# Kernel tuning notes

Hardware: AMD Instinct MI355X
Metric: run time of the kernel (lower is better)

The kernel has to match this reference:

```python
import jax, jax.numpy as jnp
import numpy as np

N_NODES = 50000


def setup_inputs() -> dict:
    key = jax.random.key(0)
    k1, k2, k3 = jax.random.split(key, 3)
    x = jax.random.normal(k1, (N_NODES, 256), dtype=jnp.float32)
    edge_index = jax.random.randint(k2, (2, 1600000), 0, N_NODES, dtype=jnp.int64)
    W = jax.random.normal(k3, (256, 256), dtype=jnp.float32) / np.sqrt(256.0)
    b = jnp.zeros((256,), dtype=jnp.float32)
    return {"x": x, "edge_index": edge_index, "W": W, "b": b}


def reference(x, edge_index, W, b):
    # PyG GCNConv: add self-loops, symmetric normalization, linear, aggregate, bias; then ReLU.
    n = x.shape[0]
    self_loops = jnp.arange(n, dtype=edge_index.dtype)
    src = jnp.concatenate([edge_index[0], self_loops])  # [E+N]
    dst = jnp.concatenate([edge_index[1], self_loops])  # [E+N]

    # degree from incoming edges (incl. self loops)
    deg = jax.ops.segment_sum(jnp.ones_like(dst, dtype=x.dtype), dst, num_segments=n)
    dinv = jnp.where(deg > 0, jax.lax.rsqrt(deg), 0.0)
    norm = dinv[src] * dinv[dst]  # [E+N]

    xw = x @ W  # [N, out] linear first (GCNConv transforms then propagates)
    msgs = xw[src] * norm[:, None]  # gather + edge-normalize
    agg = jax.ops.segment_sum(msgs, dst, num_segments=n)  # scatter-add
    return jax.nn.relu(agg + b)
```

## Files before the change

kernel.cpp:

```cpp
#include <hip/hip_runtime.h>
#include <hip/hip_bf16.h>


#define FEATS 256
#define MAXBUCK 200
#define P1_CAP 64
#define BCAP 10240

typedef __bf16 bf16x8 __attribute__((ext_vector_type(8)));
typedef float f32x4 __attribute__((ext_vector_type(4)));

__device__ __forceinline__ unsigned short f2bf(float f) {
  unsigned u = __float_as_uint(f);
  u += 0x7fffu + ((u >> 16) & 1u);
  return (unsigned short)(u >> 16);
}
__device__ __forceinline__ float bflo(unsigned u) { return __uint_as_float(u << 16); }
__device__ __forceinline__ float bfhi(unsigned u) { return __uint_as_float(u & 0xFFFF0000u); }


__global__ __launch_bounds__(256) void zero_i32(int* __restrict__ p, int n) {
  int i = blockIdx.x * 256 + threadIdx.x;
  if (i < n) p[i] = 0;
}

__global__ __launch_bounds__(1024) void pass1_bin(const int* __restrict__ src,
                                                  const int* __restrict__ dst,
                                                  int E, int nbuck,
                                                  int* __restrict__ gcursor,
                                                  unsigned* __restrict__ temp) {
  __shared__ unsigned lbuf[MAXBUCK * P1_CAP];
  __shared__ int lcnt[MAXBUCK];
  __shared__ int lbase[MAXBUCK];
  const int tid = threadIdx.x;
  for (int i = tid; i < nbuck; i += 1024) lcnt[i] = 0;
  __syncthreads();

  const int e0 = blockIdx.x * 4096;
  #pragma unroll
  for (int i = 0; i < 4; ++i) {
    int e = e0 + i * 1024 + tid;
    if (e < E) {
      unsigned d = (unsigned)dst[e];
      unsigned p = (d << 16) | (unsigned)src[e];
      int b = (int)(d >> 8);
      int pos = atomicAdd(&lcnt[b], 1);
      if (pos < P1_CAP) {
        lbuf[b * P1_CAP + pos] = p;
      } else {
        int gp = atomicAdd(&gcursor[b], 1);
        temp[(size_t)b * BCAP + gp] = p;
      }
    }
  }
  __syncthreads();
  if (tid < nbuck) {
    int c = lcnt[tid]; if (c > P1_CAP) c = P1_CAP;
    lcnt[tid] = c;
    lbase[tid] = atomicAdd(&gcursor[tid], c);
  }
  __syncthreads();
  for (int i = tid; i < nbuck * P1_CAP; i += 1024) {
    int b = i >> 6, j = i & (P1_CAP - 1);
    if (j < lcnt[b]) temp[(size_t)b * BCAP + lbase[b] + j] = lbuf[i];
  }
}

__global__ __launch_bounds__(256) void scan_buckets(const int* __restrict__ gcursor,
                                                    int* __restrict__ bbase,
                                                    int* __restrict__ row_ptr,
                                                    int nbuck, int n) {
  __shared__ int tmp[256];
  int t = threadIdx.x;
  int v = (t < nbuck) ? min(gcursor[t], BCAP) : 0;
  tmp[t] = v;
  __syncthreads();
  #pragma unroll
  for (int off = 1; off < 256; off <<= 1) {
    int x = (t >= off) ? tmp[t - off] : 0;
    __syncthreads();
    tmp[t] += x;
    __syncthreads();
  }
  if (t < nbuck) bbase[t] = tmp[t] - v;
  if (t == 0) row_ptr[n] = tmp[255];
}

__global__ __launch_bounds__(1024) void pass2_csr(const unsigned* __restrict__ temp,
                                                  const int* __restrict__ gcursor,
                                                  const int* __restrict__ bbase,
                                                  unsigned short* __restrict__ csr16,
                                                  int* __restrict__ row_ptr,
                                                  float* __restrict__ dinv, int n) {
  __shared__ unsigned ebuf[BCAP];
  __shared__ unsigned short sorted[BCAP];
  __shared__ int hist[256], scn[256], sexcl[256], ofs[256];
  const int b = blockIdx.x;
  const int tid = threadIdx.x;
  int cnt = gcursor[b]; if (cnt > BCAP) cnt = BCAP;
  const int base = bbase[b];
  const unsigned* tp = temp + (size_t)b * BCAP;

  if (tid < 256) { hist[tid] = 0; ofs[tid] = 0; }
  for (int i = tid; i < cnt; i += 1024) ebuf[i] = tp[i];
  __syncthreads();
  for (int i = tid; i < cnt; i += 1024) atomicAdd(&hist[(ebuf[i] >> 16) & 255], 1);
  __syncthreads();

  if (tid < 256) scn[tid] = hist[tid];
  __syncthreads();
  #pragma unroll
  for (int off = 1; off < 256; off <<= 1) {
    int x = 0;
    if (tid < 256 && tid >= off) x = scn[tid - off];
    __syncthreads();
    if (tid < 256) scn[tid] += x;
    __syncthreads();
  }
  if (tid < 256) {
    int v = hist[tid];
    int excl = scn[tid] - v;
    sexcl[tid] = excl;
    int node = (b << 8) + tid;
    if (node < n) {
      row_ptr[node] = base + excl;
      dinv[node] = rsqrtf((float)(v + 1));
    }
  }
  __syncthreads();

  for (int i = tid; i < cnt; i += 1024) {
    unsigned e = ebuf[i];
    int dl = (int)((e >> 16) & 255);
    int pos = sexcl[dl] + atomicAdd(&ofs[dl], 1);
    sorted[pos] = (unsigned short)(e & 0xFFFFu);
  }
  __syncthreads();
  for (int i = tid; i < cnt; i += 1024) csr16[base + i] = sorted[i];
}


__global__ __launch_bounds__(256) void wt_build(const float* __restrict__ W,
                                                unsigned short* __restrict__ Wt) {
  int k = blockIdx.x;
  int nn = threadIdx.x;
  Wt[nn * FEATS + k] = f2bf(W[k * FEATS + nn]);
}


__global__ __launch_bounds__(256, 2) void gemm_mfma(const float* __restrict__ x,
                                                    const unsigned short* __restrict__ Wt,
                                                    const float* __restrict__ dinv,
                                                    unsigned short* __restrict__ xwp, int M) {
  __shared__ bf16x8 A_lds[32 * 64];
  __shared__ unsigned short C_lds[64 * 256];
  const int wv   = (int)(threadIdx.x >> 6);
  const int lane = (int)(threadIdx.x & 63);
  const int lm   = lane & 15;
  const int quad = lane >> 4;
  const int m0   = (int)blockIdx.x * 64;

  bf16x8 Bfrag[4][8];
  #pragma unroll
  for (int ct = 0; ct < 4; ++ct) {
    const unsigned short* wrow = Wt + (size_t)(wv * 64 + ct * 16 + lm) * FEATS + quad * 8;
    #pragma unroll
    for (int kc = 0; kc < 8; ++kc)
      Bfrag[ct][kc] = *(const bf16x8*)(wrow + kc * 32);
  }

  {
    int arow = m0 + wv * 16 + lm; if (arow >= M) arow = M - 1;
    const float* xrow = x + (size_t)arow * FEATS + quad * 8;
    #pragma unroll
    for (int kc = 0; kc < 8; ++kc) {
      const float4 f0 = *(const float4*)(xrow + kc * 32);
      const float4 f1 = *(const float4*)(xrow + kc * 32 + 4);
      union { bf16x8 v; unsigned short u[8]; } a;
      a.u[0] = f2bf(f0.x); a.u[1] = f2bf(f0.y); a.u[2] = f2bf(f0.z); a.u[3] = f2bf(f0.w);
      a.u[4] = f2bf(f1.x); a.u[5] = f2bf(f1.y); a.u[6] = f2bf(f1.z); a.u[7] = f2bf(f1.w);
      A_lds[(wv * 8 + kc) * 64 + lane] = a.v;
    }
  }
  __syncthreads();

  #pragma unroll
  for (int sub = 0; sub < 4; ++sub) {
    bf16x8 Af[8];
    #pragma unroll
    for (int kc = 0; kc < 8; ++kc) Af[kc] = A_lds[(sub * 8 + kc) * 64 + lane];

    f32x4 acc[4];
    #pragma unroll
    for (int ct = 0; ct < 4; ++ct) acc[ct] = (f32x4){0.f, 0.f, 0.f, 0.f};

    #pragma unroll
    for (int kc = 0; kc < 8; ++kc) {
      #pragma unroll
      for (int ct = 0; ct < 4; ++ct)
        acc[ct] = __builtin_amdgcn_mfma_f32_16x16x32_bf16(Af[kc], Bfrag[ct][kc], acc[ct], 0, 0, 0);
    }

    #pragma unroll
    for (int r = 0; r < 4; ++r) {
      const int lrow = sub * 16 + quad * 4 + r;
      int grow = m0 + lrow; if (grow >= M) grow = M - 1;
      const float dd = dinv[grow];
      #pragma unroll
      for (int ct = 0; ct < 4; ++ct)
        C_lds[lrow * 256 + wv * 64 + ((ct ^ quad) << 4) + lm] = f2bf(acc[ct][r] * dd);
    }
  }
  __syncthreads();

  const int t  = (int)(threadIdx.x & 31);
  const int r8 = (int)(threadIdx.x >> 5);
  #pragma unroll
  for (int j = 0; j < 8; ++j) {
    const int lrow = j * 8 + r8;
    const int grow = m0 + lrow;
    if (grow < M) {
      const int qr = (lrow >> 2) & 3;
      const unsigned short* srcp = C_lds + lrow * 256 + (((t * 16) ^ (qr << 5)) >> 1);
      *(uint4*)(xwp + (size_t)grow * FEATS + t * 8) = *(const uint4*)srcp;
    }
  }
}


__global__ __launch_bounds__(256) void aggregate(const unsigned short* __restrict__ xwp,
                                                 const float* __restrict__ dinv,
                                                 const int* __restrict__ row_ptr,
                                                 const unsigned short* __restrict__ csr16,
                                                 const float* __restrict__ bias,
                                                 float* __restrict__ out,
                                                 int n0, int n1) {
  const int node = n0 + (int)((blockIdx.x * blockDim.x + threadIdx.x) >> 6);
  const int lane = (int)(threadIdx.x & 63);
  if (node >= n1) return;
  const int co = lane << 2;

  uint2 sv = *(const uint2*)(xwp + (((size_t)node) << 8) + co);
  float4 acc;
  acc.x = bflo(sv.x); acc.y = bfhi(sv.x); acc.z = bflo(sv.y); acc.w = bfhi(sv.y);

  const int beg = row_ptr[node];
  const int end = row_ptr[node + 1];
  for (int base = beg; base < end; base += 64) {
    int idx = base + lane;
    int s = (idx < end) ? (int)csr16[idx] : 0;
    int m = end - base;
    if (m > 64) m = 64;
    int i = 0;
    for (; i + 8 <= m; i += 8) {
      uint2 v[8];
      #pragma unroll
      for (int j = 0; j < 8; ++j) {
        int sj = __shfl(s, i + j);
        v[j] = *(const uint2*)(xwp + (((size_t)sj) << 8) + co);
      }
      #pragma unroll
      for (int j = 0; j < 8; ++j) {
        acc.x += bflo(v[j].x); acc.y += bfhi(v[j].x);
        acc.z += bflo(v[j].y); acc.w += bfhi(v[j].y);
      }
    }
    for (; i < m; ++i) {
      int sj = __shfl(s, i);
      uint2 v = *(const uint2*)(xwp + (((size_t)sj) << 8) + co);
      acc.x += bflo(v.x); acc.y += bfhi(v.x);
      acc.z += bflo(v.y); acc.w += bfhi(v.y);
    }
  }

  const float dd = dinv[node];
  const float* bp = bias + co;
  f32x4 o;
  o.x = fmaxf(fmaf(acc.x, dd, bp[0]), 0.f);
  o.y = fmaxf(fmaf(acc.y, dd, bp[1]), 0.f);
  o.z = fmaxf(fmaf(acc.z, dd, bp[2]), 0.f);
  o.w = fmaxf(fmaf(acc.w, dd, bp[3]), 0.f);
  __builtin_nontemporal_store(o, (f32x4*)(out + (((size_t)node) << 8) + co));
}


extern "C" void kernel_launch(void* const* d_in, const int* in_sizes, int n_in,
                              void* d_out, int out_size, void* d_ws, size_t ws_size,
                              hipStream_t stream) {
  const float* x  = (const float*)d_in[0];
  const int*   ei = (const int*)d_in[1];
  const float* W  = (const float*)d_in[2];
  const float* b  = (const float*)d_in[3];

  const int n = in_sizes[0] / FEATS;
  const int E = in_sizes[1] / 2;
  const int* src = ei;
  const int* dst = ei + E;
  const int nbuck = (n + 255) >> 8;

  char* ws = (char*)d_ws;
  size_t o0 = 0;
  unsigned short* xwp    = (unsigned short*)(ws + o0); o0 += (size_t)n * 512;
  unsigned short* Wt     = (unsigned short*)(ws + o0); o0 += 131072;
  float*          dinv   = (float*)(ws + o0);          o0 += 200064;
  int*            row_ptr = (int*)(ws + o0);           o0 += 200064;
  unsigned short* csr16  = (unsigned short*)(ws + o0); o0 += 3200000;
  int*            gcursor = (int*)(ws + o0);           o0 += 1024;
  int*            bbase   = (int*)(ws + o0);           o0 += 1024;
  unsigned*       temp    = (unsigned*)(ws + o0);      o0 += (size_t)MAXBUCK * BCAP * 4;

  hipLaunchKernelGGL(zero_i32, dim3(1), dim3(256), 0, stream, gcursor, nbuck);
  hipLaunchKernelGGL(wt_build, dim3(256), dim3(256), 0, stream, W, Wt);

  const int g_p1 = (E + 4095) / 4096;
  hipLaunchKernelGGL(pass1_bin, dim3(g_p1), dim3(1024), 0, stream, src, dst, E, nbuck, gcursor, temp);
  hipLaunchKernelGGL(scan_buckets, dim3(1), dim3(256), 0, stream, gcursor, bbase, row_ptr, nbuck, n);
  hipLaunchKernelGGL(pass2_csr, dim3(nbuck), dim3(1024), 0, stream, temp, gcursor, bbase,
                     csr16, row_ptr, dinv, n);

  hipLaunchKernelGGL(gemm_mfma, dim3((n + 63) / 64), dim3(256), 0, stream, x, Wt, dinv, xwp, n);

  const int nh = (n + 1) >> 1;
  const int g_agg = (nh * 64 + 255) / 256;
  hipLaunchKernelGGL(aggregate, dim3(g_agg), dim3(256), 0, stream,
                     xwp, dinv, row_ptr, csr16, b, (float*)d_out, 0, nh);
  hipLaunchKernelGGL(aggregate, dim3(g_agg), dim3(256), 0, stream,
                     xwp, dinv, row_ptr, csr16, b, (float*)d_out, nh, n);
}
```

Baseline: 258.6 us.

## Gather two neighbor rows per wave with 16-byte loads and merge init kernels

The aggregate kernel now splits each wave into two 32-lane halves that each load a full 256-feature bf16 row with 16-byte loads, so one wave processes two edges per step. The halves are combined with a cross-half shuffle reduction. Out-of-range slots point at an extra zeroed padding row so loads need no branch. The zero and weight-transpose kernels are merged into one launch, and the two half-range aggregate launches become one. This aims to cut load instruction count and launch overhead, at the cost of extra shuffles, more registers and wasted loads on partial edge groups.

```diff
diff --git a/kernel.cpp b/kernel.cpp
--- a/kernel.cpp
+++ b/kernel.cpp
@@ -18,11 +18,6 @@
 __device__ __forceinline__ float bflo(unsigned u) { return __uint_as_float(u << 16); }
 __device__ __forceinline__ float bfhi(unsigned u) { return __uint_as_float(u & 0xFFFF0000u); }
 
-
-__global__ __launch_bounds__(256) void zero_i32(int* __restrict__ p, int n) {
-  int i = blockIdx.x * 256 + threadIdx.x;
-  if (i < n) p[i] = 0;
-}
 
 __global__ __launch_bounds__(1024) void pass1_bin(const int* __restrict__ src,
                                                   const int* __restrict__ dst,
@@ -140,11 +135,18 @@
 }
 
 
-__global__ __launch_bounds__(256) void wt_build(const float* __restrict__ W,
-                                                unsigned short* __restrict__ Wt) {
-  int k = blockIdx.x;
-  int nn = threadIdx.x;
-  Wt[nn * FEATS + k] = f2bf(W[k * FEATS + nn]);
+__global__ __launch_bounds__(256) void wt_init(const float* __restrict__ W,
+                                               unsigned short* __restrict__ Wt,
+                                               int* __restrict__ gcursor, int nbuck,
+                                               unsigned* __restrict__ xwp_srow) {
+  const int bk = (int)blockIdx.x;
+  const int t  = (int)threadIdx.x;
+  if (bk < 256) {
+    Wt[t * FEATS + bk] = f2bf(W[bk * FEATS + t]);
+  } else {
+    if (t < nbuck) gcursor[t] = 0;
+    if (t < 128) xwp_srow[t] = 0;
+  }
 }
 
 
@@ -228,59 +230,75 @@
 }
 
 
+#define AGG_ACC(J0, CNT) do {                                                      \
+    uint4 vv[CNT];                                                                 \
+    _Pragma("unroll")                                                              \
+    for (int j = 0; j < (CNT); ++j) {                                              \
+      int sj = __shfl(s, (J0) + 2 * j + half);                                     \
+      vv[j] = *(const uint4*)(xb + ((size_t)sj << 8));                             \
+    }                                                                              \
+    _Pragma("unroll")                                                              \
+    for (int j = 0; j < (CNT); ++j) {                                              \
+      a0 += bflo(vv[j].x); a1 += bfhi(vv[j].x);                                    \
+      a2 += bflo(vv[j].y); a3 += bfhi(vv[j].y);                                    \
+      a4 += bflo(vv[j].z); a5 += bfhi(vv[j].z);                                    \
+      a6 += bflo(vv[j].w); a7 += bfhi(vv[j].w);                                    \
+    }                                                                              \
+  } while (0)
+
 __global__ __launch_bounds__(256) void aggregate(const unsigned short* __restrict__ xwp,
                                                  const float* __restrict__ dinv,
                                                  const int* __restrict__ row_ptr,
                                                  const unsigned short* __restrict__ csr16,
                                                  const float* __restrict__ bias,
-                                                 float* __restrict__ out,
-                                                 int n0, int n1) {
-  const int node = n0 + (int)((blockIdx.x * blockDim.x + threadIdx.x) >> 6);
+                                                 float* __restrict__ out, int n) {
+  const int node = (int)((blockIdx.x * blockDim.x + threadIdx.x) >> 6);
   const int lane = (int)(threadIdx.x & 63);
-  if (node >= n1) return;
-  const int co = lane << 2;
-
-  uint2 sv = *(const uint2*)(xwp + (((size_t)node) << 8) + co);
-  float4 acc;
-  acc.x = bflo(sv.x); acc.y = bfhi(sv.x); acc.z = bflo(sv.y); acc.w = bfhi(sv.y);
+  if (node >= n) return;
+  const int half = lane >> 5;
+  const int cl   = lane & 31;
+  const unsigned short* xb = xwp + cl * 8;
+
+  float a0 = 0.f, a1 = 0.f, a2 = 0.f, a3 = 0.f, a4 = 0.f, a5 = 0.f, a6 = 0.f, a7 = 0.f;
+  {
+    uint4 v = *(const uint4*)(xb + ((size_t)node << 8));
+    if (half == 0) {
+      a0 = bflo(v.x); a1 = bfhi(v.x); a2 = bflo(v.y); a3 = bfhi(v.y);
+      a4 = bflo(v.z); a5 = bfhi(v.z); a6 = bflo(v.w); a7 = bfhi(v.w);
+    }
+  }
 
   const int beg = row_ptr[node];
   const int end = row_ptr[node + 1];
   for (int base = beg; base < end; base += 64) {
     int idx = base + lane;
-    int s = (idx < end) ? (int)csr16[idx] : 0;
-    int m = end - base;
-    if (m > 64) m = 64;
+    int s = (idx < end) ? (int)csr16[idx] : n;
+    int m = end - base; if (m > 64) m = 64;
     int i = 0;
-    for (; i + 8 <= m; i += 8) {
-      uint2 v[8];
-      #pragma unroll
-      for (int j = 0; j < 8; ++j) {
-        int sj = __shfl(s, i + j);
-        v[j] = *(const uint2*)(xwp + (((size_t)sj) << 8) + co);
-      }
-      #pragma unroll
-      for (int j = 0; j < 8; ++j) {
-        acc.x += bflo(v[j].x); acc.y += bfhi(v[j].x);
-        acc.z += bflo(v[j].y); acc.w += bfhi(v[j].y);
-      }
-    }
-    for (; i < m; ++i) {
-      int sj = __shfl(s, i);
-      uint2 v = *(const uint2*)(xwp + (((size_t)sj) << 8) + co);
-      acc.x += bflo(v.x); acc.y += bfhi(v.x);
-      acc.z += bflo(v.y); acc.w += bfhi(v.y);
-    }
-  }
-
+    for (; i + 16 <= m; i += 16) AGG_ACC(i, 8);
+    if (i < m) {
+      if (m - i <= 8) AGG_ACC(i, 4);
+      else            AGG_ACC(i, 8);
+    }
+  }
+
+  a0 += __shfl_xor(a0, 32); a1 += __shfl_xor(a1, 32);
+  a2 += __shfl_xor(a2, 32); a3 += __shfl_xor(a3, 32);
+  a4 += __shfl_xor(a4, 32); a5 += __shfl_xor(a5, 32);
+  a6 += __shfl_xor(a6, 32); a7 += __shfl_xor(a7, 32);
+
+  const float s0 = half ? a4 : a0;
+  const float s1 = half ? a5 : a1;
+  const float s2 = half ? a6 : a2;
+  const float s3 = half ? a7 : a3;
   const float dd = dinv[node];
-  const float* bp = bias + co;
+  const float* bp = bias + cl * 8 + half * 4;
   f32x4 o;
-  o.x = fmaxf(fmaf(acc.x, dd, bp[0]), 0.f);
-  o.y = fmaxf(fmaf(acc.y, dd, bp[1]), 0.f);
-  o.z = fmaxf(fmaf(acc.z, dd, bp[2]), 0.f);
-  o.w = fmaxf(fmaf(acc.w, dd, bp[3]), 0.f);
-  __builtin_nontemporal_store(o, (f32x4*)(out + (((size_t)node) << 8) + co));
+  o.x = fmaxf(fmaf(s0, dd, bp[0]), 0.f);
+  o.y = fmaxf(fmaf(s1, dd, bp[1]), 0.f);
+  o.z = fmaxf(fmaf(s2, dd, bp[2]), 0.f);
+  o.w = fmaxf(fmaf(s3, dd, bp[3]), 0.f);
+  __builtin_nontemporal_store(o, (f32x4*)(out + (size_t)node * 256 + cl * 8 + half * 4));
 }
 
 
@@ -300,7 +318,7 @@
 
   char* ws = (char*)d_ws;
   size_t o0 = 0;
-  unsigned short* xwp    = (unsigned short*)(ws + o0); o0 += (size_t)n * 512;
+  unsigned short* xwp    = (unsigned short*)(ws + o0); o0 += (size_t)(n + 1) * 512;
   unsigned short* Wt     = (unsigned short*)(ws + o0); o0 += 131072;
   float*          dinv   = (float*)(ws + o0);          o0 += 200064;
   int*            row_ptr = (int*)(ws + o0);           o0 += 200064;
@@ -309,8 +327,8 @@
   int*            bbase   = (int*)(ws + o0);           o0 += 1024;
   unsigned*       temp    = (unsigned*)(ws + o0);      o0 += (size_t)MAXBUCK * BCAP * 4;
 
-  hipLaunchKernelGGL(zero_i32, dim3(1), dim3(256), 0, stream, gcursor, nbuck);
-  hipLaunchKernelGGL(wt_build, dim3(256), dim3(256), 0, stream, W, Wt);
+  hipLaunchKernelGGL(wt_init, dim3(257), dim3(256), 0, stream, W, Wt, gcursor, nbuck,
+                     (unsigned*)(xwp + (size_t)n * 256));
 
   const int g_p1 = (E + 4095) / 4096;
   hipLaunchKernelGGL(pass1_bin, dim3(g_p1), dim3(1024), 0, stream, src, dst, E, nbuck, gcursor, temp);
@@ -320,10 +338,7 @@
 
   hipLaunchKernelGGL(gemm_mfma, dim3((n + 63) / 64), dim3(256), 0, stream, x, Wt, dinv, xwp, n);
 
-  const int nh = (n + 1) >> 1;
-  const int g_agg = (nh * 64 + 255) / 256;
+  const int g_agg = (n * 64 + 255) / 256;
   hipLaunchKernelGGL(aggregate, dim3(g_agg), dim3(256), 0, stream,
-                     xwp, dinv, row_ptr, csr16, b, (float*)d_out, 0, nh);
-  hipLaunchKernelGGL(aggregate, dim3(g_agg), dim3(256), 0, stream,
-                     xwp, dinv, row_ptr, csr16, b, (float*)d_out, nh, n);
-}
+                     xwp, dinv, row_ptr, csr16, b, (float*)d_out, n);
+}
```

Result: faster. 251.9 us (-2.6%).
